# Kernel tuning notes

Measured on AMD Instinct MI355X. Metric: run time of the kernel, lower is better.

Reference implementation:

```python
import jax, jax.numpy as jnp
import numpy as np

TEMPERATURE = 0.5

def setup_inputs() -> dict:
    key = jax.random.key(0)
    k1, k2 = jax.random.split(key)
    N, D = 4096, 256
    z1 = jax.random.normal(k1, (N, D), dtype=jnp.float32)
    z2 = jax.random.normal(k2, (N, D), dtype=jnp.float32)
    return {"z1": z1, "z2": z2}

def reference(z1, z2):
    N, D = z1.shape
    # Interleave rows: Z[::2] = z1, Z[1::2] = z2  -> shape (2N, D)
    Z = jnp.stack([z1, z2], axis=1).reshape(2 * N, D).astype(jnp.float32)
    # L2 normalize rows (torch F.normalize default eps=1e-12)
    Z = Z / jnp.maximum(jnp.linalg.norm(Z, axis=1, keepdims=True), 1e-12)
    # Dense exp-similarity matrix (2N, 2N)
    S = jnp.exp(jnp.matmul(Z, Z.T) / TEMPERATURE)
    idx = jnp.arange(2 * N)
    diag = jnp.diagonal(S)
    rowsum = jnp.sum(S, axis=1)
    # positive pair of row i is row i^1 (2i <-> 2i+1)
    pos = S[idx, idx ^ 1]
    loss_per_row = -jnp.log(pos / (rowsum - diag + 1e-8))
    return jnp.sum(loss_per_row) / (2 * N)
```

## Files before the change

kernel.cpp:

```cpp
#include <hip/hip_runtime.h>
#include <hip/hip_bf16.h>
#include <stdint.h>

#define N2 8192
#define D 256
#define DB 512
#define RB_ROWS 256
#define WAVE_ROWS 32
#define CHUNK 32
#define JSPLIT 16
#define COLS_PER_BLOCK (N2 / JSPLIT)
#define CHUNKS_PER_BLOCK (COLS_PER_BLOCK / CHUNK)
#define SWZ(r, b) ((b) ^ (((r) & 7) << 4))

using short8 = __attribute__((ext_vector_type(8))) short;
using f32x4  = __attribute__((ext_vector_type(4))) float;

typedef __attribute__((address_space(1))) const char gchar_t;
typedef __attribute__((address_space(3))) char       lchar_t;

__device__ inline unsigned short f2bf(float x) {
    union { float f; uint32_t u; } a; a.f = x;
    uint32_t r = (a.u + 0x7fff + ((a.u >> 16) & 1)) >> 16;
    return (unsigned short)r;
}

__global__ void knorm(const float* __restrict__ z1, const float* __restrict__ z2,
                      unsigned short* __restrict__ Zb, float* __restrict__ den) {
    int tid  = threadIdx.x;
    int lane = tid & 63;
    int w    = tid >> 6;
    int row  = blockIdx.x * 4 + w;
    const float* src = (row & 1) ? z2 : z1;
    int srow = row >> 1;
    float4 v = reinterpret_cast<const float4*>(src + (size_t)srow * D)[lane];
    float ss = v.x*v.x + v.y*v.y + v.z*v.z + v.w*v.w;
    #pragma unroll
    for (int off = 1; off < 64; off <<= 1) ss += __shfl_xor(ss, off);
    float inv = rsqrtf(ss);
    ushort4 o;
    o.x = f2bf(v.x * inv); o.y = f2bf(v.y * inv);
    o.z = f2bf(v.z * inv); o.w = f2bf(v.w * inv);
    *reinterpret_cast<ushort4*>(Zb + (size_t)row * D + lane * 4) = o;

    int gid = blockIdx.x * blockDim.x + tid;
    if (gid < N2) den[gid] = 0.f;
}

__launch_bounds__(512, 4)
__global__ void kmain(const unsigned short* __restrict__ Zb,
                      float* __restrict__ den, float* __restrict__ pos) {
    __shared__ char tile[2][CHUNK * DB];
    int tid  = threadIdx.x;
    int lane = tid & 63;
    int w    = tid >> 6;
    int bid  = blockIdx.x;
    int rb   = bid & 31;
    int js   = bid >> 5;
    int Rw   = rb * RB_ROWS + w * WAVE_ROWS;
    int Cbase = js * COLS_PER_BLOCK;
    int l15 = lane & 15, g = lane >> 4;

    const char* Zc = reinterpret_cast<const char*>(Zb);

    short8 A[2][8];
    #pragma unroll
    for (int mf = 0; mf < 2; ++mf) {
        const char* rowp = Zc + (size_t)(Rw + mf*16 + l15) * DB + g*16;
        #pragma unroll
        for (int s = 0; s < 8; ++s)
            A[mf][s] = *reinterpret_cast<const short8*>(rowp + s*64);
    }

    int soff[2];
    #pragma unroll
    for (int k = 0; k < 2; ++k) {
        int r = w*4 + k*2 + (lane >> 5);
        int y = (lane & 31) * 16;
        soff[k] = r * DB + SWZ(r, y);
    }

    float rsum[2][4];
    #pragma unroll
    for (int mf = 0; mf < 2; ++mf)
        #pragma unroll
        for (int r = 0; r < 4; ++r) rsum[mf][r] = 0.f;

    const size_t cb0 = (size_t)Cbase * DB;

    #define STAGE(bf, coff)                                                          \
        __builtin_amdgcn_global_load_lds(                                            \
            (gchar_t*)(Zc + (coff) + soff[0]),                                       \
            (lchar_t*)(&tile[bf][(w*4 + 0) * DB]), 16, 0, 0);                        \
        __builtin_amdgcn_global_load_lds(                                            \
            (gchar_t*)(Zc + (coff) + soff[1]),                                       \
            (lchar_t*)(&tile[bf][(w*4 + 2) * DB]), 16, 0, 0);

    STAGE(0, cb0);
    int buf = 0;

    for (int c = 0; c < CHUNKS_PER_BLOCK; ++c) {
        if (c + 1 < CHUNKS_PER_BLOCK) {
            STAGE(buf ^ 1, cb0 + (size_t)(c + 1) * CHUNK * DB);
            asm volatile("s_waitcnt vmcnt(2)" ::: "memory");
        } else {
            asm volatile("s_waitcnt vmcnt(0)" ::: "memory");
        }
        __builtin_amdgcn_s_barrier();
        __builtin_amdgcn_sched_barrier(0);

        f32x4 acc[2][2];
        #pragma unroll
        for (int mf = 0; mf < 2; ++mf)
            #pragma unroll
            for (int nf = 0; nf < 2; ++nf) acc[mf][nf] = (f32x4){0.f,0.f,0.f,0.f};

        #pragma unroll
        for (int s = 0; s < 8; ++s) {
            int cb = s*64 + g*16;
            int r0 = l15, r1 = 16 + l15;
            short8 B0 = *reinterpret_cast<const short8*>(&tile[buf][r0 * DB + SWZ(r0, cb)]);
            short8 B1 = *reinterpret_cast<const short8*>(&tile[buf][r1 * DB + SWZ(r1, cb)]);
            #pragma unroll
            for (int mf = 0; mf < 2; ++mf) {
                acc[mf][0] = __builtin_amdgcn_mfma_f32_16x16x32_bf16(A[mf][s], B0, acc[mf][0], 0, 0, 0);
                acc[mf][1] = __builtin_amdgcn_mfma_f32_16x16x32_bf16(A[mf][s], B1, acc[mf][1], 0, 0, 0);
            }
        }

        int C0 = Cbase + c * CHUNK;
        #pragma unroll
        for (int mf = 0; mf < 2; ++mf) {
            int Rt = Rw + mf * 16;
            #pragma unroll
            for (int nf = 0; nf < 2; ++nf) {
                int Ct = C0 + nf * 16;
                bool dg = (Ct == Rt);
                #pragma unroll
                for (int r = 0; r < 4; ++r) {
                    float v = acc[mf][nf][r];
                    float e = exp2f(v * 2.885390081777927f);
                    if (dg) {
                        int rl = g * 4 + r;
                        if (l15 == rl) e = 0.f;
                        if (l15 == (rl ^ 1)) pos[Rt + rl] = v;
                    }
                    rsum[mf][r] += e;
                }
            }
        }
        __builtin_amdgcn_sched_barrier(0);
        __builtin_amdgcn_s_barrier();
        buf ^= 1;
    }

    #pragma unroll
    for (int mf = 0; mf < 2; ++mf) {
        #pragma unroll
        for (int r = 0; r < 4; ++r) {
            float v = rsum[mf][r];
            v += __shfl_xor(v, 1); v += __shfl_xor(v, 2);
            v += __shfl_xor(v, 4); v += __shfl_xor(v, 8);
            if (l15 == 0) atomicAdd(&den[Rw + mf*16 + g*4 + r], v);
        }
    }
}

__global__ void kloss(const float* __restrict__ den, const float* __restrict__ pos,
                      float* __restrict__ out) {
    __shared__ float red[4];
    int tid = threadIdx.x;
    int idx = blockIdx.x * 256 + tid;
    float s = logf(den[idx] + 1e-8f) - 2.f * pos[idx];
    #pragma unroll
    for (int off = 1; off < 64; off <<= 1) s += __shfl_xor(s, off);
    if ((tid & 63) == 0) red[tid >> 6] = s;
    __syncthreads();
    if (tid == 0)
        atomicAdd(out, (red[0] + red[1] + red[2] + red[3]) * (1.f / (float)N2));
}

extern "C" void kernel_launch(void* const* d_in, const int* in_sizes, int n_in,
                              void* d_out, int out_size, void* d_ws, size_t ws_size,
                              hipStream_t stream) {
    const float* z1 = (const float*)d_in[0];
    const float* z2 = (const float*)d_in[1];
    char* ws = (char*)d_ws;
    unsigned short* Zb = (unsigned short*)ws;
    float* den = (float*)(ws + (size_t)N2 * DB);
    float* pos = (float*)(ws + (size_t)N2 * DB + (size_t)N2 * 4);

    hipMemsetAsync(d_out, 0, sizeof(float), stream);
    knorm<<<N2 / 4, 256, 0, stream>>>(z1, z2, Zb, den);
    kmain<<<32 * JSPLIT, 512, 0, stream>>>(Zb, den, pos);
    kloss<<<N2 / 256, 256, 0, stream>>>(den, pos, (float*)d_out);
}
```

Measured before the change: 104.5 us.

## Double rows per wave, fuse loss reduction into last block, drop memset

Each wave now holds 64 A rows instead of 32, so every B tile loaded into LDS feeds twice as many MFMAs. The grid shrinks to 256 blocks with launch bounds set for 2 blocks per CU. The separate loss kernel and the output memset are removed; the last block, found through an atomic counter, computes the final log-sum reduction. The explicit vmcnt waits are replaced with __syncthreads. This trades register pressure and occupancy for less LDS traffic and fewer launches, and the grid of 256 blocks may underfill the CUs.

```diff
diff --git a/kernel.cpp b/kernel.cpp
--- a/kernel.cpp
+++ b/kernel.cpp
@@ -5,12 +5,13 @@
 #define N2 8192
 #define D 256
 #define DB 512
-#define RB_ROWS 256
-#define WAVE_ROWS 32
+#define BLK_ROWS 512
+#define WAVE_ROWS 64
 #define CHUNK 32
 #define JSPLIT 16
 #define COLS_PER_BLOCK (N2 / JSPLIT)
 #define CHUNKS_PER_BLOCK (COLS_PER_BLOCK / CHUNK)
+#define NBLOCKS (16 * JSPLIT)
 #define SWZ(r, b) ((b) ^ (((r) & 7) << 4))
 
 using short8 = __attribute__((ext_vector_type(8))) short;
@@ -26,7 +27,8 @@
 }
 
 __global__ void knorm(const float* __restrict__ z1, const float* __restrict__ z2,
-                      unsigned short* __restrict__ Zb, float* __restrict__ den) {
+                      unsigned short* __restrict__ Zb, float* __restrict__ den,
+                      int* __restrict__ counter) {
     int tid  = threadIdx.x;
     int lane = tid & 63;
     int w    = tid >> 6;
@@ -45,32 +47,25 @@
 
     int gid = blockIdx.x * blockDim.x + tid;
     if (gid < N2) den[gid] = 0.f;
-}
-
-__launch_bounds__(512, 4)
+    if (gid == 0) *counter = 0;
+}
+
+__launch_bounds__(512, 2)
 __global__ void kmain(const unsigned short* __restrict__ Zb,
-                      float* __restrict__ den, float* __restrict__ pos) {
+                      float* __restrict__ den, float* __restrict__ pos,
+                      int* __restrict__ counter, float* __restrict__ out) {
     __shared__ char tile[2][CHUNK * DB];
     int tid  = threadIdx.x;
     int lane = tid & 63;
     int w    = tid >> 6;
     int bid  = blockIdx.x;
-    int rb   = bid & 31;
-    int js   = bid >> 5;
-    int Rw   = rb * RB_ROWS + w * WAVE_ROWS;
+    int rb   = bid & 15;
+    int js   = bid >> 4;
+    int Rw   = rb * BLK_ROWS + w * WAVE_ROWS;
     int Cbase = js * COLS_PER_BLOCK;
     int l15 = lane & 15, g = lane >> 4;
 
     const char* Zc = reinterpret_cast<const char*>(Zb);
-
-    short8 A[2][8];
-    #pragma unroll
-    for (int mf = 0; mf < 2; ++mf) {
-        const char* rowp = Zc + (size_t)(Rw + mf*16 + l15) * DB + g*16;
-        #pragma unroll
-        for (int s = 0; s < 8; ++s)
-            A[mf][s] = *reinterpret_cast<const short8*>(rowp + s*64);
-    }
 
     int soff[2];
     #pragma unroll
@@ -79,13 +74,6 @@
         int y = (lane & 31) * 16;
         soff[k] = r * DB + SWZ(r, y);
     }
-
-    float rsum[2][4];
-    #pragma unroll
-    for (int mf = 0; mf < 2; ++mf)
-        #pragma unroll
-        for (int r = 0; r < 4; ++r) rsum[mf][r] = 0.f;
-
     const size_t cb0 = (size_t)Cbase * DB;
 
     #define STAGE(bf, coff)                                                          \
@@ -97,21 +85,32 @@
             (lchar_t*)(&tile[bf][(w*4 + 2) * DB]), 16, 0, 0);
 
     STAGE(0, cb0);
+
+    short8 A[4][8];
+    #pragma unroll
+    for (int mf = 0; mf < 4; ++mf) {
+        const char* rowp = Zc + (size_t)(Rw + mf*16 + l15) * DB + g*16;
+        #pragma unroll
+        for (int s = 0; s < 8; ++s)
+            A[mf][s] = *reinterpret_cast<const short8*>(rowp + s*64);
+    }
+
+    float rsum[4][4];
+    #pragma unroll
+    for (int mf = 0; mf < 4; ++mf)
+        #pragma unroll
+        for (int r = 0; r < 4; ++r) rsum[mf][r] = 0.f;
+
+    __syncthreads();
     int buf = 0;
 
     for (int c = 0; c < CHUNKS_PER_BLOCK; ++c) {
-        if (c + 1 < CHUNKS_PER_BLOCK) {
+        if (c + 1 < CHUNKS_PER_BLOCK)
             STAGE(buf ^ 1, cb0 + (size_t)(c + 1) * CHUNK * DB);
-            asm volatile("s_waitcnt vmcnt(2)" ::: "memory");
-        } else {
-            asm volatile("s_waitcnt vmcnt(0)" ::: "memory");
-        }
-        __builtin_amdgcn_s_barrier();
-        __builtin_amdgcn_sched_barrier(0);
-
-        f32x4 acc[2][2];
-        #pragma unroll
-        for (int mf = 0; mf < 2; ++mf)
+
+        f32x4 acc[4][2];
+        #pragma unroll
+        for (int mf = 0; mf < 4; ++mf)
             #pragma unroll
             for (int nf = 0; nf < 2; ++nf) acc[mf][nf] = (f32x4){0.f,0.f,0.f,0.f};
 
@@ -122,7 +121,7 @@
             short8 B0 = *reinterpret_cast<const short8*>(&tile[buf][r0 * DB + SWZ(r0, cb)]);
             short8 B1 = *reinterpret_cast<const short8*>(&tile[buf][r1 * DB + SWZ(r1, cb)]);
             #pragma unroll
-            for (int mf = 0; mf < 2; ++mf) {
+            for (int mf = 0; mf < 4; ++mf) {
                 acc[mf][0] = __builtin_amdgcn_mfma_f32_16x16x32_bf16(A[mf][s], B0, acc[mf][0], 0, 0, 0);
                 acc[mf][1] = __builtin_amdgcn_mfma_f32_16x16x32_bf16(A[mf][s], B1, acc[mf][1], 0, 0, 0);
             }
@@ -130,7 +129,7 @@
 
         int C0 = Cbase + c * CHUNK;
         #pragma unroll
-        for (int mf = 0; mf < 2; ++mf) {
+        for (int mf = 0; mf < 4; ++mf) {
             int Rt = Rw + mf * 16;
             #pragma unroll
             for (int nf = 0; nf < 2; ++nf) {
@@ -149,13 +148,12 @@
                 }
             }
         }
-        __builtin_amdgcn_sched_barrier(0);
-        __builtin_amdgcn_s_barrier();
+        __syncthreads();
         buf ^= 1;
     }
 
     #pragma unroll
-    for (int mf = 0; mf < 2; ++mf) {
+    for (int mf = 0; mf < 4; ++mf) {
         #pragma unroll
         for (int r = 0; r < 4; ++r) {
             float v = rsum[mf][r];
@@ -164,20 +162,32 @@
             if (l15 == 0) atomicAdd(&den[Rw + mf*16 + g*4 + r], v);
         }
     }
-}
-
-__global__ void kloss(const float* __restrict__ den, const float* __restrict__ pos,
-                      float* __restrict__ out) {
-    __shared__ float red[4];
-    int tid = threadIdx.x;
-    int idx = blockIdx.x * 256 + tid;
-    float s = logf(den[idx] + 1e-8f) - 2.f * pos[idx];
+
+    __shared__ int  amLast;
+    __shared__ float red[8];
+    __threadfence();
+    __syncthreads();
+    if (tid == 0) amLast = (atomicAdd(counter, 1) == NBLOCKS - 1);
+    __syncthreads();
+    if (!amLast) return;
+    __threadfence();
+
+    float s = 0.f;
+    for (int i = tid; i < N2; i += 512) {
+        float d = __hip_atomic_load(&den[i], __ATOMIC_RELAXED, __HIP_MEMORY_SCOPE_AGENT);
+        float p = __hip_atomic_load(&pos[i], __ATOMIC_RELAXED, __HIP_MEMORY_SCOPE_AGENT);
+        s += logf(d + 1e-8f) - 2.f * p;
+    }
     #pragma unroll
     for (int off = 1; off < 64; off <<= 1) s += __shfl_xor(s, off);
-    if ((tid & 63) == 0) red[tid >> 6] = s;
-    __syncthreads();
-    if (tid == 0)
-        atomicAdd(out, (red[0] + red[1] + red[2] + red[3]) * (1.f / (float)N2));
+    if (lane == 0) red[w] = s;
+    __syncthreads();
+    if (tid == 0) {
+        float t = 0.f;
+        #pragma unroll
+        for (int i = 0; i < 8; ++i) t += red[i];
+        out[0] = t * (1.f / (float)N2);
+    }
 }
 
 extern "C" void kernel_launch(void* const* d_in, const int* in_sizes, int n_in,
@@ -189,9 +199,8 @@
     unsigned short* Zb = (unsigned short*)ws;
     float* den = (float*)(ws + (size_t)N2 * DB);
     float* pos = (float*)(ws + (size_t)N2 * DB + (size_t)N2 * 4);
-
-    hipMemsetAsync(d_out, 0, sizeof(float), stream);
-    knorm<<<N2 / 4, 256, 0, stream>>>(z1, z2, Zb, den);
-    kmain<<<32 * JSPLIT, 512, 0, stream>>>(Zb, den, pos);
-    kloss<<<N2 / 256, 256, 0, stream>>>(den, pos, (float*)d_out);
-}
+    int* counter = (int*)(ws + (size_t)N2 * DB + (size_t)N2 * 8);
+
+    knorm<<<N2 / 4, 256, 0, stream>>>(z1, z2, Zb, den, counter);
+    kmain<<<NBLOCKS, 512, 0, stream>>>(Zb, den, pos, counter, (float*)d_out);
+}
```

Measured after the change: 145.7 us. +39.5%, slower.
